# Kernel optimization log

Hardware: AMD Instinct MI355X
Metric: run time of the kernel (lower is better)

## Reference

```python
import jax, jax.numpy as jnp
import numpy as np

D_MODEL = 256
NHEAD = 8
HEAD_DIM = D_MODEL // NHEAD
CLIP = 10.0


def setup_inputs() -> dict:
    key = jax.random.key(0)
    k1, k2, k3, k4 = jax.random.split(key, 4)
    B, N = 4, 256
    nodes = jax.random.normal(k1, (B, N, D_MODEL), dtype=jnp.float32)
    edges = jax.random.normal(k2, (B, N, N, D_MODEL), dtype=jnp.float32)
    # torch nn.Linear default init: U(-1/sqrt(in), 1/sqrt(in))
    bound = 1.0 / np.sqrt(D_MODEL)
    W = jax.random.uniform(k3, (D_MODEL, D_MODEL), minval=-bound, maxval=bound, dtype=jnp.float32)
    b = jax.random.uniform(k4, (D_MODEL,), minval=-bound, maxval=bound, dtype=jnp.float32)
    return {"nodes": nodes, "edges": edges, "W": W, "b": b}


def reference(nodes, edges, W, b):
    B, N, _ = nodes.shape
    H, Dh = NHEAD, HEAD_DIM

    def proj(x):  # torch Linear: x @ W.T + b
        return x @ W.T + b

    # Node projections: the module applies the SAME linear to q, k, v
    node_p = proj(nodes).reshape(B, N, H, Dh)
    nq, nk, nv = node_p, node_p, node_p
    # Edge projections (same linear for q and k)
    edge_p = proj(edges).reshape(B, N, N, H, Dh)
    eq, ek = edge_p, edge_p

    query = eq + nq[:, :, None, :, :]   # (B,N,N,H,Dh)
    key = ek + nk[:, None, :, :, :]     # (B,N,N,H,Dh)
    scores = jnp.einsum('bijhd,bijhd->bhij', query, key) / np.sqrt(Dh).astype(np.float32)
    scores = CLIP * jnp.tanh(scores)
    attn = jax.nn.softmax(scores, axis=-1)  # (B,H,N,N)
    # output = attn @ values (values transposed to (B,H,N,Dh))
    out = jnp.einsum('bhij,bjhd->bihd', attn, nv).reshape(B, N, D_MODEL)
    out = proj(out)
    return (out, attn)
```

## Files before the change

### kernel.cpp

```cpp
#include <hip/hip_runtime.h>
#include <hip/hip_bf16.h>
#include <math.h>

typedef short short8 __attribute__((ext_vector_type(8)));
typedef float f32x4 __attribute__((ext_vector_type(4)));

__device__ __forceinline__ unsigned short f2bf(float x) {
    unsigned u = __float_as_uint(x);
    u += 0x7FFF + ((u >> 16) & 1);
    return (unsigned short)(u >> 16);
}
__device__ __forceinline__ float bf2f(unsigned short h) {
    return __uint_as_float(((unsigned)h) << 16);
}

__device__ __forceinline__ void cvt2(float f0, float f1,
                                     unsigned short& h0, unsigned short& h1,
                                     unsigned short& l0, unsigned short& l1) {
    __hip_bfloat162 h = __float22bfloat162_rn(float2{f0, f1});
    unsigned hu = *(unsigned*)&h;
    h0 = (unsigned short)(hu & 0xFFFFu);
    h1 = (unsigned short)(hu >> 16);
    float r0 = f0 - __uint_as_float((hu & 0xFFFFu) << 16);
    float r1 = f1 - __uint_as_float(hu & 0xFFFF0000u);
    __hip_bfloat162 lo = __float22bfloat162_rn(float2{r0, r1});
    unsigned lu = *(unsigned*)&lo;
    l0 = (unsigned short)(lu & 0xFFFFu);
    l1 = (unsigned short)(lu >> 16);
}

__device__ __forceinline__ float tanh10(float y) {
    float e = __expf(2.f * y);
    return 10.f * (e - 1.f) / (e + 1.f);
}

#define GLDS16(gp, lp)                                                        \
    __builtin_amdgcn_global_load_lds(                                         \
        (const __attribute__((address_space(1))) void*)(gp),                  \
        (__attribute__((address_space(3))) void*)(lp), 16, 0, 0)

__global__ __launch_bounds__(256) void k_prep(const float* __restrict__ W,
                                              float* __restrict__ Wt,
                                              unsigned short* __restrict__ Whi,
                                              unsigned short* __restrict__ Wlo) {
    int d = blockIdx.x, k = threadIdx.x;
    float w = W[d * 256 + k];
    Wt[k * 256 + d] = w;
    unsigned short hi = f2bf(w);
    Whi[d * 256 + k] = hi;
    Wlo[d * 256 + k] = f2bf(w - bf2f(hi));
}

__global__ __launch_bounds__(256) void k_node_proj(const float* __restrict__ nodes,
                                                   const float* __restrict__ Wt,
                                                   const float* __restrict__ bias,
                                                   float* __restrict__ np_) {
    int row = blockIdx.x;
    int d = threadIdx.x;
    __shared__ float xl[256];
    xl[d] = nodes[row * 256 + d];
    __syncthreads();
    float a[8] = {0.f, 0.f, 0.f, 0.f, 0.f, 0.f, 0.f, 0.f};
#pragma unroll 4
    for (int k = 0; k < 256; k += 8) {
#pragma unroll
        for (int q = 0; q < 8; ++q)
            a[q] = fmaf(xl[k + q], Wt[(k + q) * 256 + d], a[q]);
    }
    np_[row * 256 + d] =
        bias[d] + ((a[0] + a[1]) + (a[2] + a[3])) + ((a[4] + a[5]) + (a[6] + a[7]));
}

__global__ __launch_bounds__(256) void k_edge_mfma(const float* __restrict__ edges,
                                                   const unsigned short* __restrict__ Whi,
                                                   const unsigned short* __restrict__ Wlo,
                                                   const float* __restrict__ bias,
                                                   const float* __restrict__ np_,
                                                   float* __restrict__ attn) {
    __shared__ unsigned short Eh[128 * 32], El[128 * 32];
    __shared__ unsigned short Wh[128 * 32], Wl[128 * 32];
    __shared__ float npi[128];
    __shared__ float sc[4][128];

    const int t = threadIdx.x;
    const int w = t >> 6, l = t & 63;
    const int tile = blockIdx.x >> 1;
    const int half = blockIdx.x & 1;
    const int m0 = tile * 128;
    const int bb = m0 >> 16;
    const int ii = (m0 >> 8) & 255;
    const int j0 = m0 & 255;
    const int n0 = half * 128;

    if (t < 32)
        ((float4*)npi)[t] = ((const float4*)(np_ + (size_t)(bb * 256 + ii) * 256 + n0))[t];

    f32x4 acc[4][4];
#pragma unroll
    for (int mt = 0; mt < 4; ++mt)
#pragma unroll
        for (int nt = 0; nt < 4; ++nt) acc[mt][nt] = (f32x4){0.f, 0.f, 0.f, 0.f};

    const int er = t >> 1, ehk = t & 1;
    const float* esrc = edges + (size_t)(m0 + er) * 256 + ehk * 16;

    const int wrow = (l >> 2), wq = l & 3;

    const int col = l & 15, g = l >> 4;
    const int wm = (w & 1) * 64, wn = (w >> 1) * 64;

    float4 ecur[4], enext[4];
#pragma unroll
    for (int q = 0; q < 4; ++q) ecur[q] = *(const float4*)(esrc + q * 4);

    for (int kc = 0; kc < 8; ++kc) {
#pragma unroll
        for (int s = 0; s < 2; ++s) {
            int base = w * 32 + s * 16;
            const unsigned short* gh =
                Whi + (size_t)(n0 + base + wrow) * 256 + kc * 32 + wq * 8;
            const unsigned short* gl =
                Wlo + (size_t)(n0 + base + wrow) * 256 + kc * 32 + wq * 8;
            GLDS16(gh, Wh + base * 32);
            GLDS16(gl, Wl + base * 32);
        }
        {
            unsigned short hi[16], lo[16];
#pragma unroll
            for (int q = 0; q < 4; ++q) {
                cvt2(ecur[q].x, ecur[q].y, hi[q * 4 + 0], hi[q * 4 + 1],
                     lo[q * 4 + 0], lo[q * 4 + 1]);
                cvt2(ecur[q].z, ecur[q].w, hi[q * 4 + 2], hi[q * 4 + 3],
                     lo[q * 4 + 2], lo[q * 4 + 3]);
            }
            *(short8*)(Eh + er * 32 + ehk * 16)     = *(short8*)&hi[0];
            *(short8*)(Eh + er * 32 + ehk * 16 + 8) = *(short8*)&hi[8];
            *(short8*)(El + er * 32 + ehk * 16)     = *(short8*)&lo[0];
            *(short8*)(El + er * 32 + ehk * 16 + 8) = *(short8*)&lo[8];
        }
        if (kc < 7) {
#pragma unroll
            for (int q = 0; q < 4; ++q)
                enext[q] = *(const float4*)(esrc + (kc + 1) * 32 + q * 4);
        }
        __syncthreads();
        short8 Ah[4], Al[4];
#pragma unroll
        for (int mt = 0; mt < 4; ++mt) {
            Ah[mt] = *(const short8*)(Eh + (wm + mt * 16 + col) * 32 + g * 8);
            Al[mt] = *(const short8*)(El + (wm + mt * 16 + col) * 32 + g * 8);
        }
#pragma unroll
        for (int nt = 0; nt < 4; ++nt) {
            short8 Bh = *(const short8*)(Wh + (wn + nt * 16 + col) * 32 + g * 8);
            short8 Bl = *(const short8*)(Wl + (wn + nt * 16 + col) * 32 + g * 8);
#pragma unroll
            for (int mt = 0; mt < 4; ++mt) {
                acc[mt][nt] = __builtin_amdgcn_mfma_f32_16x16x32_bf16(Ah[mt], Bh, acc[mt][nt], 0, 0, 0);
                acc[mt][nt] = __builtin_amdgcn_mfma_f32_16x16x32_bf16(Ah[mt], Bl, acc[mt][nt], 0, 0, 0);
                acc[mt][nt] = __builtin_amdgcn_mfma_f32_16x16x32_bf16(Al[mt], Bh, acc[mt][nt], 0, 0, 0);
            }
        }
        __syncthreads();
#pragma unroll
        for (int q = 0; q < 4; ++q) ecur[q] = enext[q];
    }

    const float isq = 0.17677669529663687f;
    float bv[4], nv[4];
#pragma unroll
    for (int nt = 0; nt < 4; ++nt) {
        int dl = wn + nt * 16 + col;
        bv[nt] = bias[n0 + dl];
        nv[nt] = npi[dl];
    }
    const int hl0 = (w >> 1) * 2;
#pragma unroll
    for (int mt = 0; mt < 4; ++mt) {
#pragma unroll
        for (int r = 0; r < 4; ++r) {
            int el = wm + mt * 16 + g * 4 + r;
            int j = j0 + el;
            const float* npj = np_ + (size_t)(bb * 256 + j) * 256 + n0 + wn;
            float p0 = acc[mt][0][r] + bv[0];
            float p1 = acc[mt][1][r] + bv[1];
            float p2 = acc[mt][2][r] + bv[2];
            float p3 = acc[mt][3][r] + bv[3];
            float s0 = (p0 + nv[0]) * (p0 + npj[col]) +
                       (p1 + nv[1]) * (p1 + npj[16 + col]);
            float s1 = (p2 + nv[2]) * (p2 + npj[32 + col]) +
                       (p3 + nv[3]) * (p3 + npj[48 + col]);
#pragma unroll
            for (int m = 1; m < 16; m <<= 1) {
                s0 += __shfl_xor(s0, m, 64);
                s1 += __shfl_xor(s1, m, 64);
            }
            if (col == 0) {
                sc[hl0][el]     = tanh10(s0 * isq);
                sc[hl0 + 1][el] = tanh10(s1 * isq);
            }
        }
    }
    __syncthreads();
    if (t < 128) {
        int hl = t >> 5, q = t & 31;
        float4 v = *(float4*)&sc[hl][q * 4];
        *(float4*)(attn + (((size_t)(bb * 8 + half * 4 + hl) * 256 + ii) << 8) + j0 + q * 4) = v;
    }
}

__global__ __launch_bounds__(256) void k_softmax(float* __restrict__ attn) {
    int row = (blockIdx.x * 256 + threadIdx.x) >> 6;
    int lane = threadIdx.x & 63;
    float4* rowp = (float4*)(attn + (size_t)row * 256);
    float4 v = rowp[lane];
    float m = fmaxf(fmaxf(v.x, v.y), fmaxf(v.z, v.w));
#pragma unroll
    for (int s = 1; s < 64; s <<= 1) m = fmaxf(m, __shfl_xor(m, s, 64));
    v.x = __expf(v.x - m); v.y = __expf(v.y - m);
    v.z = __expf(v.z - m); v.w = __expf(v.w - m);
    float sum = v.x + v.y + v.z + v.w;
#pragma unroll
    for (int s = 1; s < 64; s <<= 1) sum += __shfl_xor(sum, s, 64);
    float inv = 1.f / sum;
    v.x *= inv; v.y *= inv; v.z *= inv; v.w *= inv;
    rowp[lane] = v;
}

__global__ __launch_bounds__(256) void k_out(const float* __restrict__ attn,
                                             const float* __restrict__ np_,
                                             const float* __restrict__ Wt,
                                             const float* __restrict__ bias,
                                             float* __restrict__ out) {
    int bi = blockIdx.x;
    int bb = bi >> 8, ii = bi & 255;
    int d = threadIdx.x;
    __shared__ float at[8 * 256];
    __shared__ float xl[256];
#pragma unroll
    for (int s = 0; s < 2; ++s) {
        int idx = d + s * 256;
        int h = idx >> 6, q = idx & 63;
        ((float4*)at)[idx] =
            ((const float4*)(attn + ((size_t)(bb * 8 + h) * 256 + ii) * 256))[q];
    }
    __syncthreads();
    int h = d >> 5;
    const float* npb = np_ + (size_t)bb * 65536 + d;
    const float* ath = at + h * 256;
    float a[8] = {0.f, 0.f, 0.f, 0.f, 0.f, 0.f, 0.f, 0.f};
#pragma unroll 2
    for (int j = 0; j < 256; j += 8) {
#pragma unroll
        for (int q = 0; q < 8; ++q)
            a[q] = fmaf(ath[j + q], npb[(size_t)(j + q) * 256], a[q]);
    }
    xl[d] = ((a[0] + a[1]) + (a[2] + a[3])) + ((a[4] + a[5]) + (a[6] + a[7]));
    __syncthreads();
    float c[8] = {bias[d], 0.f, 0.f, 0.f, 0.f, 0.f, 0.f, 0.f};
#pragma unroll 2
    for (int k = 0; k < 256; k += 8) {
#pragma unroll
        for (int q = 0; q < 8; ++q)
            c[q] = fmaf(xl[k + q], Wt[(k + q) * 256 + d], c[q]);
    }
    out[bi * 256 + d] =
        ((c[0] + c[1]) + (c[2] + c[3])) + ((c[4] + c[5]) + (c[6] + c[7]));
}

extern "C" void kernel_launch(void* const* d_in, const int* in_sizes, int n_in,
                              void* d_out, int out_size, void* d_ws, size_t ws_size,
                              hipStream_t stream) {
    (void)in_sizes; (void)n_in; (void)out_size; (void)ws_size;
    const float* nodes = (const float*)d_in[0];
    const float* edges = (const float*)d_in[1];
    const float* W     = (const float*)d_in[2];
    const float* bias  = (const float*)d_in[3];

    float* out  = (float*)d_out;
    float* attn = out + 262144;

    float* np_ = (float*)d_ws;
    float* Wt  = np_ + 262144;
    unsigned short* Whi = (unsigned short*)(Wt + 65536);
    unsigned short* Wlo = Whi + 65536;

    hipLaunchKernelGGL(k_prep,      dim3(256),  dim3(256), 0, stream, W, Wt, Whi, Wlo);
    hipLaunchKernelGGL(k_node_proj, dim3(1024), dim3(256), 0, stream, nodes, Wt, bias, np_);
    hipLaunchKernelGGL(k_edge_mfma, dim3(4096), dim3(256), 0, stream, edges, Whi, Wlo, bias, np_, attn);
    hipLaunchKernelGGL(k_softmax,   dim3(2048), dim3(256), 0, stream, attn);
    hipLaunchKernelGGL(k_out,       dim3(1024), dim3(256), 0, stream, attn, np_, Wt, bias, out);
}
```

Baseline: 529.6 us.

## Drop LDS staging in edge GEMM, full-N tiles per block, fuse softmax into output

```diff
diff --git a/kernel.cpp b/kernel.cpp
--- a/kernel.cpp
+++ b/kernel.cpp
@@ -14,30 +14,27 @@
     return __uint_as_float(((unsigned)h) << 16);
 }
 
-__device__ __forceinline__ void cvt2(float f0, float f1,
-                                     unsigned short& h0, unsigned short& h1,
-                                     unsigned short& l0, unsigned short& l1) {
-    __hip_bfloat162 h = __float22bfloat162_rn(float2{f0, f1});
-    unsigned hu = *(unsigned*)&h;
-    h0 = (unsigned short)(hu & 0xFFFFu);
-    h1 = (unsigned short)(hu >> 16);
-    float r0 = f0 - __uint_as_float((hu & 0xFFFFu) << 16);
-    float r1 = f1 - __uint_as_float(hu & 0xFFFF0000u);
-    __hip_bfloat162 lo = __float22bfloat162_rn(float2{r0, r1});
-    unsigned lu = *(unsigned*)&lo;
-    l0 = (unsigned short)(lu & 0xFFFFu);
-    l1 = (unsigned short)(lu >> 16);
+__device__ __forceinline__ void cvt8(const float4 a, const float4 b,
+                                     short8& hi, short8& lo) {
+    float f[8] = {a.x, a.y, a.z, a.w, b.x, b.y, b.z, b.w};
+    unsigned hu[4], lu[4];
+#pragma unroll
+    for (int p = 0; p < 4; ++p) {
+        __hip_bfloat162 h = __float22bfloat162_rn(float2{f[2 * p], f[2 * p + 1]});
+        hu[p] = *(unsigned*)&h;
+        float r0 = f[2 * p]     - __uint_as_float(hu[p] << 16);
+        float r1 = f[2 * p + 1] - __uint_as_float(hu[p] & 0xFFFF0000u);
+        __hip_bfloat162 lo2 = __float22bfloat162_rn(float2{r0, r1});
+        lu[p] = *(unsigned*)&lo2;
+    }
+    hi = *(short8*)hu;
+    lo = *(short8*)lu;
 }
 
 __device__ __forceinline__ float tanh10(float y) {
     float e = __expf(2.f * y);
     return 10.f * (e - 1.f) / (e + 1.f);
 }
-
-#define GLDS16(gp, lp)                                                        \
-    __builtin_amdgcn_global_load_lds(                                         \
-        (const __attribute__((address_space(1))) void*)(gp),                  \
-        (__attribute__((address_space(3))) void*)(lp), 16, 0, 0)
 
 __global__ __launch_bounds__(256) void k_prep(const float* __restrict__ W,
                                               float* __restrict__ Wt,
@@ -77,174 +74,146 @@
                                                    const float* __restrict__ bias,
                                                    const float* __restrict__ np_,
                                                    float* __restrict__ attn) {
-    __shared__ unsigned short Eh[128 * 32], El[128 * 32];
-    __shared__ unsigned short Wh[128 * 32], Wl[128 * 32];
-    __shared__ float npi[128];
-    __shared__ float sc[4][128];
+    __shared__ float sc[8][64];
 
     const int t = threadIdx.x;
     const int w = t >> 6, l = t & 63;
-    const int tile = blockIdx.x >> 1;
-    const int half = blockIdx.x & 1;
-    const int m0 = tile * 128;
+    const int col = l & 15, g = l >> 4;
+    const int m0 = blockIdx.x * 64;
     const int bb = m0 >> 16;
     const int ii = (m0 >> 8) & 255;
     const int j0 = m0 & 255;
-    const int n0 = half * 128;
-
-    if (t < 32)
-        ((float4*)npi)[t] = ((const float4*)(np_ + (size_t)(bb * 256 + ii) * 256 + n0))[t];
-
-    f32x4 acc[4][4];
-#pragma unroll
-    for (int mt = 0; mt < 4; ++mt)
-#pragma unroll
-        for (int nt = 0; nt < 4; ++nt) acc[mt][nt] = (f32x4){0.f, 0.f, 0.f, 0.f};
-
-    const int er = t >> 1, ehk = t & 1;
-    const float* esrc = edges + (size_t)(m0 + er) * 256 + ehk * 16;
-
-    const int wrow = (l >> 2), wq = l & 3;
-
-    const int col = l & 15, g = l >> 4;
-    const int wm = (w & 1) * 64, wn = (w >> 1) * 64;
-
-    float4 ecur[4], enext[4];
-#pragma unroll
-    for (int q = 0; q < 4; ++q) ecur[q] = *(const float4*)(esrc + q * 4);
+    const int wm = (w & 1) * 32;
+    const int wn = (w >> 1) * 128;
+
+    f32x4 acc[2][8];
+#pragma unroll
+    for (int mt = 0; mt < 2; ++mt)
+#pragma unroll
+        for (int nt = 0; nt < 8; ++nt) acc[mt][nt] = (f32x4){0.f, 0.f, 0.f, 0.f};
+
+    const float* arow = edges + (size_t)(m0 + wm + col) * 256 + g * 8;
+    const unsigned short* bh0 = Whi + (size_t)(wn + col) * 256 + g * 8;
+    const unsigned short* bl0 = Wlo + (size_t)(wn + col) * 256 + g * 8;
+
+    float4 ac[2][2], an[2][2];
+#pragma unroll
+    for (int mt = 0; mt < 2; ++mt) {
+        ac[mt][0] = *(const float4*)(arow + mt * 4096);
+        ac[mt][1] = *(const float4*)(arow + mt * 4096 + 4);
+    }
 
     for (int kc = 0; kc < 8; ++kc) {
-#pragma unroll
-        for (int s = 0; s < 2; ++s) {
-            int base = w * 32 + s * 16;
-            const unsigned short* gh =
-                Whi + (size_t)(n0 + base + wrow) * 256 + kc * 32 + wq * 8;
-            const unsigned short* gl =
-                Wlo + (size_t)(n0 + base + wrow) * 256 + kc * 32 + wq * 8;
-            GLDS16(gh, Wh + base * 32);
-            GLDS16(gl, Wl + base * 32);
-        }
-        {
-            unsigned short hi[16], lo[16];
-#pragma unroll
-            for (int q = 0; q < 4; ++q) {
-                cvt2(ecur[q].x, ecur[q].y, hi[q * 4 + 0], hi[q * 4 + 1],
-                     lo[q * 4 + 0], lo[q * 4 + 1]);
-                cvt2(ecur[q].z, ecur[q].w, hi[q * 4 + 2], hi[q * 4 + 3],
-                     lo[q * 4 + 2], lo[q * 4 + 3]);
-            }
-            *(short8*)(Eh + er * 32 + ehk * 16)     = *(short8*)&hi[0];
-            *(short8*)(Eh + er * 32 + ehk * 16 + 8) = *(short8*)&hi[8];
-            *(short8*)(El + er * 32 + ehk * 16)     = *(short8*)&lo[0];
-            *(short8*)(El + er * 32 + ehk * 16 + 8) = *(short8*)&lo[8];
-        }
         if (kc < 7) {
 #pragma unroll
-            for (int q = 0; q < 4; ++q)
-                enext[q] = *(const float4*)(esrc + (kc + 1) * 32 + q * 4);
-        }
-        __syncthreads();
-        short8 Ah[4], Al[4];
-#pragma unroll
-        for (int mt = 0; mt < 4; ++mt) {
-            Ah[mt] = *(const short8*)(Eh + (wm + mt * 16 + col) * 32 + g * 8);
-            Al[mt] = *(const short8*)(El + (wm + mt * 16 + col) * 32 + g * 8);
-        }
-#pragma unroll
-        for (int nt = 0; nt < 4; ++nt) {
-            short8 Bh = *(const short8*)(Wh + (wn + nt * 16 + col) * 32 + g * 8);
-            short8 Bl = *(const short8*)(Wl + (wn + nt * 16 + col) * 32 + g * 8);
-#pragma unroll
-            for (int mt = 0; mt < 4; ++mt) {
-                acc[mt][nt] = __builtin_amdgcn_mfma_f32_16x16x32_bf16(Ah[mt], Bh, acc[mt][nt], 0, 0, 0);
-                acc[mt][nt] = __builtin_amdgcn_mfma_f32_16x16x32_bf16(Ah[mt], Bl, acc[mt][nt], 0, 0, 0);
-                acc[mt][nt] = __builtin_amdgcn_mfma_f32_16x16x32_bf16(Al[mt], Bh, acc[mt][nt], 0, 0, 0);
-            }
-        }
-        __syncthreads();
-#pragma unroll
-        for (int q = 0; q < 4; ++q) ecur[q] = enext[q];
+            for (int mt = 0; mt < 2; ++mt) {
+                an[mt][0] = *(const float4*)(arow + mt * 4096 + (kc + 1) * 32);
+                an[mt][1] = *(const float4*)(arow + mt * 4096 + (kc + 1) * 32 + 4);
+            }
+        }
+        short8 Bh[8], Bl[8];
+#pragma unroll
+        for (int nt = 0; nt < 8; ++nt) {
+            Bh[nt] = *(const short8*)(bh0 + (size_t)nt * 4096 + kc * 32);
+            Bl[nt] = *(const short8*)(bl0 + (size_t)nt * 4096 + kc * 32);
+        }
+        short8 Ah[2], Al[2];
+#pragma unroll
+        for (int mt = 0; mt < 2; ++mt) cvt8(ac[mt][0], ac[mt][1], Ah[mt], Al[mt]);
+#pragma unroll
+        for (int nt = 0; nt < 8; ++nt)
+#pragma unroll
+            for (int mt = 0; mt < 2; ++mt) {
+                acc[mt][nt] = __builtin_amdgcn_mfma_f32_16x16x32_bf16(Ah[mt], Bh[nt], acc[mt][nt], 0, 0, 0);
+                acc[mt][nt] = __builtin_amdgcn_mfma_f32_16x16x32_bf16(Ah[mt], Bl[nt], acc[mt][nt], 0, 0, 0);
+                acc[mt][nt] = __builtin_amdgcn_mfma_f32_16x16x32_bf16(Al[mt], Bh[nt], acc[mt][nt], 0, 0, 0);
+            }
+#pragma unroll
+        for (int mt = 0; mt < 2; ++mt) {
+            ac[mt][0] = an[mt][0];
+            ac[mt][1] = an[mt][1];
+        }
     }
 
     const float isq = 0.17677669529663687f;
-    float bv[4], nv[4];
-#pragma unroll
-    for (int nt = 0; nt < 4; ++nt) {
-        int dl = wn + nt * 16 + col;
-        bv[nt] = bias[n0 + dl];
-        nv[nt] = npi[dl];
-    }
-    const int hl0 = (w >> 1) * 2;
-#pragma unroll
-    for (int mt = 0; mt < 4; ++mt) {
+    float bv[8], nv[8];
+    const float* npi = np_ + (size_t)(bb * 256 + ii) * 256 + wn;
+#pragma unroll
+    for (int nt = 0; nt < 8; ++nt) {
+        bv[nt] = bias[wn + nt * 16 + col];
+        nv[nt] = npi[nt * 16 + col];
+    }
+#pragma unroll
+    for (int mt = 0; mt < 2; ++mt) {
 #pragma unroll
         for (int r = 0; r < 4; ++r) {
             int el = wm + mt * 16 + g * 4 + r;
             int j = j0 + el;
-            const float* npj = np_ + (size_t)(bb * 256 + j) * 256 + n0 + wn;
-            float p0 = acc[mt][0][r] + bv[0];
-            float p1 = acc[mt][1][r] + bv[1];
-            float p2 = acc[mt][2][r] + bv[2];
-            float p3 = acc[mt][3][r] + bv[3];
-            float s0 = (p0 + nv[0]) * (p0 + npj[col]) +
-                       (p1 + nv[1]) * (p1 + npj[16 + col]);
-            float s1 = (p2 + nv[2]) * (p2 + npj[32 + col]) +
-                       (p3 + nv[3]) * (p3 + npj[48 + col]);
+            const float* npj = np_ + (size_t)(bb * 256 + j) * 256 + wn;
+            float s[4] = {0.f, 0.f, 0.f, 0.f};
+#pragma unroll
+            for (int nt = 0; nt < 8; ++nt) {
+                float p = acc[mt][nt][r] + bv[nt];
+                s[nt >> 1] += (p + nv[nt]) * (p + npj[nt * 16 + col]);
+            }
 #pragma unroll
             for (int m = 1; m < 16; m <<= 1) {
-                s0 += __shfl_xor(s0, m, 64);
-                s1 += __shfl_xor(s1, m, 64);
+#pragma unroll
+                for (int q = 0; q < 4; ++q) s[q] += __shfl_xor(s[q], m, 64);
             }
             if (col == 0) {
-                sc[hl0][el]     = tanh10(s0 * isq);
-                sc[hl0 + 1][el] = tanh10(s1 * isq);
+#pragma unroll
+                for (int q = 0; q < 4; ++q)
+                    sc[(wn >> 5) + q][el] = tanh10(s[q] * isq);
             }
         }
     }
     __syncthreads();
     if (t < 128) {
-        int hl = t >> 5, q = t & 31;
+        int hl = t >> 4, q = t & 15;
         float4 v = *(float4*)&sc[hl][q * 4];
-        *(float4*)(attn + (((size_t)(bb * 8 + half * 4 + hl) * 256 + ii) << 8) + j0 + q * 4) = v;
-    }
-}
-
-__global__ __launch_bounds__(256) void k_softmax(float* __restrict__ attn) {
-    int row = (blockIdx.x * 256 + threadIdx.x) >> 6;
-    int lane = threadIdx.x & 63;
-    float4* rowp = (float4*)(attn + (size_t)row * 256);
-    float4 v = rowp[lane];
-    float m = fmaxf(fmaxf(v.x, v.y), fmaxf(v.z, v.w));
-#pragma unroll
-    for (int s = 1; s < 64; s <<= 1) m = fmaxf(m, __shfl_xor(m, s, 64));
-    v.x = __expf(v.x - m); v.y = __expf(v.y - m);
-    v.z = __expf(v.z - m); v.w = __expf(v.w - m);
-    float sum = v.x + v.y + v.z + v.w;
-#pragma unroll
-    for (int s = 1; s < 64; s <<= 1) sum += __shfl_xor(sum, s, 64);
-    float inv = 1.f / sum;
-    v.x *= inv; v.y *= inv; v.z *= inv; v.w *= inv;
-    rowp[lane] = v;
-}
-
-__global__ __launch_bounds__(256) void k_out(const float* __restrict__ attn,
-                                             const float* __restrict__ np_,
-                                             const float* __restrict__ Wt,
-                                             const float* __restrict__ bias,
-                                             float* __restrict__ out) {
+        *(float4*)(attn + (((size_t)(bb * 8 + hl) * 256 + ii) << 8) + j0 + q * 4) = v;
+    }
+}
+
+__global__ __launch_bounds__(256) void k_smout(float* __restrict__ attn,
+                                               const float* __restrict__ np_,
+                                               const float* __restrict__ Wt,
+                                               const float* __restrict__ bias,
+                                               float* __restrict__ out) {
     int bi = blockIdx.x;
     int bb = bi >> 8, ii = bi & 255;
-    int d = threadIdx.x;
+    int t = threadIdx.x;
+    int w = t >> 6, l = t & 63;
     __shared__ float at[8 * 256];
     __shared__ float xl[256];
 #pragma unroll
     for (int s = 0; s < 2; ++s) {
-        int idx = d + s * 256;
+        int idx = t + s * 256;
         int h = idx >> 6, q = idx & 63;
         ((float4*)at)[idx] =
             ((const float4*)(attn + ((size_t)(bb * 8 + h) * 256 + ii) * 256))[q];
     }
     __syncthreads();
+#pragma unroll
+    for (int rr = 0; rr < 2; ++rr) {
+        int h = 2 * w + rr;
+        float4 v = ((float4*)(at + h * 256))[l];
+        float m = fmaxf(fmaxf(v.x, v.y), fmaxf(v.z, v.w));
+#pragma unroll
+        for (int s = 1; s < 64; s <<= 1) m = fmaxf(m, __shfl_xor(m, s, 64));
+        v.x = __expf(v.x - m); v.y = __expf(v.y - m);
+        v.z = __expf(v.z - m); v.w = __expf(v.w - m);
+        float sum = v.x + v.y + v.z + v.w;
+#pragma unroll
+        for (int s = 1; s < 64; s <<= 1) sum += __shfl_xor(sum, s, 64);
+        float inv = 1.f / sum;
+        v.x *= inv; v.y *= inv; v.z *= inv; v.w *= inv;
+        ((float4*)(at + h * 256))[l] = v;
+        ((float4*)(attn + ((size_t)(bb * 8 + h) * 256 + ii) * 256))[l] = v;
+    }
+    __syncthreads();
+    int d = t;
     int h = d >> 5;
     const float* npb = np_ + (size_t)bb * 65536 + d;
     const float* ath = at + h * 256;
@@ -288,6 +257,5 @@
     hipLaunchKernelGGL(k_prep,      dim3(256),  dim3(256), 0, stream, W, Wt, Whi, Wlo);
     hipLaunchKernelGGL(k_node_proj, dim3(1024), dim3(256), 0, stream, nodes, Wt, bias, np_);
     hipLaunchKernelGGL(k_edge_mfma, dim3(4096), dim3(256), 0, stream, edges, Whi, Wlo, bias, np_, attn);
-    hipLaunchKernelGGL(k_softmax,   dim3(2048), dim3(256), 0, stream, attn);
-    hipLaunchKernelGGL(k_out,       dim3(1024), dim3(256), 0, stream, attn, np_, Wt, bias, out);
-}
+    hipLaunchKernelGGL(k_smout,     dim3(1024), dim3(256), 0, stream, attn, np_, Wt, bias, out);
+}
```

New measurement: 643.4 us. 21.5% more time.
